# Performance work log

Hardware: AMD Instinct MI355X
Metric: run time of the kernel (lower is better)

The kernel has to match this reference:

```python
import jax, jax.numpy as jnp
import numpy as np

N = 50000      # num nodes
E = 1_600_000  # num edges
D = 64         # in_dim == hidden_dim
H = 4          # heads
C = 16         # head_dim = hidden_dim // heads
NEG = 0.2      # leaky_relu negative slope (PyG GATConv default)


def setup_inputs() -> dict:
    key = jax.random.key(0)
    ks = jax.random.split(key, 20)
    f = lambda k, s: (jax.random.normal(k, s, jnp.float32) * 0.1)
    return dict(
        node_features=jax.random.normal(ks[0], (N, D), jnp.float32),
        edge_index=jax.random.randint(ks[1], (2, E), 0, N, dtype=jnp.int32),
        edge_type=jax.random.randint(ks[2], (E,), 0, 5, dtype=jnp.int32),
        edge_attr=jax.random.normal(ks[3], (E, 1), jnp.float32),
        # GAT layer 1 (PyG GATConv: lin has no bias, att_* are [H,C], final bias [H*C])
        W1=f(ks[4], (D, H * C)), att_src1=f(ks[5], (H, C)), att_dst1=f(ks[6], (H, C)),
        We1=f(ks[7], (1, H * C)), att_e1=f(ks[8], (H, C)), b1=jnp.zeros((H * C,), jnp.float32),
        # GAT layer 2
        W2=f(ks[9], (D, H * C)), att_src2=f(ks[10], (H, C)), att_dst2=f(ks[11], (H, C)),
        We2=f(ks[12], (1, H * C)), att_e2=f(ks[13], (H, C)), b2=jnp.zeros((H * C,), jnp.float32),
        # LayerNorms
        g1=jnp.ones((D,), jnp.float32), beta1=jnp.zeros((D,), jnp.float32),
        g2=jnp.ones((D,), jnp.float32), beta2=jnp.zeros((D,), jnp.float32),
        # output head
        Wout=f(ks[14], (D, 1)), bout=jnp.zeros((1,), jnp.float32),
    )


def _layernorm(x, g, b, eps=1e-5):
    mu = x.mean(-1, keepdims=True)
    v = ((x - mu) ** 2).mean(-1, keepdims=True)
    return (x - mu) * jax.lax.rsqrt(v + eps) * g + b


def _seg_softmax(alpha, dst, n):
    # numerically stable segment softmax over incoming edges of each dst node
    m = jax.ops.segment_max(alpha, dst, num_segments=n)
    m = jnp.where(jnp.isfinite(m), m, 0.0)
    ex = jnp.exp(alpha - m[dst])
    den = jax.ops.segment_sum(ex, dst, num_segments=n)
    return ex / (den[dst] + 1e-16)


def _gatconv(x, src, dst, eattr, W, a_s, a_d, We, a_e, b, n):
    xs = (x @ W).reshape(n, H, C)                       # [N,H,C]
    a_src = jnp.einsum('nhc,hc->nh', xs, a_s)           # [N,H]
    a_dst = jnp.einsum('nhc,hc->nh', xs, a_d)           # [N,H]
    ee = (eattr @ We).reshape(-1, H, C)                 # [E',H,C]
    a_edge = jnp.einsum('ehc,hc->eh', ee, a_e)          # [E',H]
    alpha = a_src[src] + a_dst[dst] + a_edge            # [E',H]
    alpha = jax.nn.leaky_relu(alpha, NEG)
    alpha = _seg_softmax(alpha, dst, n)                 # [E',H]
    msg = xs[src] * alpha[..., None]                    # [E',H,C] gather-weighted messages
    out = jax.ops.segment_sum(msg, dst, num_segments=n) # scatter-aggregate
    return out.reshape(n, H * C) + b


def reference(node_features, edge_index, edge_type, edge_attr,
              W1, att_src1, att_dst1, We1, att_e1, b1,
              W2, att_src2, att_dst2, We2, att_e2, b2,
              g1, beta1, g2, beta2, Wout, bout):
    src, dst = edge_index[0], edge_index[1]
    # PyG add_self_loops(fill_value='mean'): self-loop edge_attr = mean of edge_attr over incoming edges
    cnt = jax.ops.segment_sum(jnp.ones((E,), jnp.float32), dst, num_segments=N)
    loop_attr = jax.ops.segment_sum(edge_attr, dst, num_segments=N) / jnp.maximum(cnt, 1.0)[:, None]
    loops = jnp.arange(N, dtype=src.dtype)
    src2 = jnp.concatenate([src, loops])
    dst2 = jnp.concatenate([dst, loops])
    ea = jnp.concatenate([edge_attr, loop_attr], axis=0)

    residual = node_features  # in_dim == hidden_dim -> no res_proj
    h = _gatconv(node_features, src2, dst2, ea, W1, att_src1, att_dst1, We1, att_e1, b1, N)
    h = jax.nn.elu(_layernorm(h + residual, g1, beta1))
    residual = h
    h = _gatconv(h, src2, dst2, ea, W2, att_src2, att_dst2, We2, att_e2, b2, N)
    h = jax.nn.elu(_layernorm(h + residual, g2, beta2))
    return h @ Wout + bout
```

## Files before the change

### kernel.cpp

```cpp
#include <hip/hip_runtime.h>
#include <hip/hip_bf16.h>
#include <cfloat>

#define NN 50000
#define NE 1600000
#define NEG 0.2f
#define NBKT 392
#define BNODE 128
#define P1_TILE 2048
#define P1_BLOCKS 782
#define CAP 16
#define BCAP 4608
#define SLOTS 96
#define L2E 1.4426950408889634f

typedef __attribute__((ext_vector_type(8))) short bf8_t;
typedef __attribute__((ext_vector_type(4))) float f4_t;

__device__ __forceinline__ float bf16bits_to_f(unsigned v) {
  return __uint_as_float(v << 16);
}
__device__ __forceinline__ unsigned f_to_bf16bits(float f) {
  unsigned u = __float_as_uint(f);
  return (u + 0x7fffu + ((u >> 16) & 1u)) >> 16;
}

__global__ __launch_bounds__(256) void bin_kernel(
    const int* __restrict__ src, const int* __restrict__ dst,
    const float* __restrict__ ea, int* __restrict__ gcnt,
    int2* __restrict__ gbuf) {
  __shared__ int lcnt[NBKT];
  __shared__ int lbase[NBKT];
  __shared__ int2 lbuf[NBKT][CAP];
  int t = threadIdx.x;
  for (int i = t; i < NBKT; i += 256) lcnt[i] = 0;
  __syncthreads();
  int e0 = blockIdx.x * P1_TILE;
#pragma unroll
  for (int k = 0; k < P1_TILE / 256; ++k) {
    int e = e0 + k * 256 + t;
    if (e < NE) {
      int d = dst[e];
      int b = d >> 7;
      int2 v = make_int2(((d & 127) << 16) | src[e], __float_as_int(ea[e]));
      int pos = atomicAdd(&lcnt[b], 1);
      if (pos < CAP) {
        lbuf[b][pos] = v;
      } else {
        int gp = atomicAdd(&gcnt[b], 1);
        if (gp < BCAP) gbuf[(size_t)b * BCAP + gp] = v;
      }
    }
  }
  __syncthreads();
  for (int i = t; i < NBKT; i += 256) {
    int len = lcnt[i]; if (len > CAP) len = CAP;
    lbase[i] = atomicAdd(&gcnt[i], len);
  }
  __syncthreads();
  for (int sid = t; sid < NBKT * CAP; sid += 256) {
    int b = sid >> 4;
    int k = sid & (CAP - 1);
    int len = lcnt[b]; if (len > CAP) len = CAP;
    if (k < len) {
      int base = lbase[b];
      if (base + k < BCAP) gbuf[(size_t)b * BCAP + base + k] = lbuf[b][k];
    }
  }
}

__global__ __launch_bounds__(256) void build_kernel(
    const int* __restrict__ gcnt, const int2* __restrict__ gbuf,
    int* __restrict__ cnt, unsigned* __restrict__ csr) {
  __shared__ int lc[BNODE];
  int t = threadIdx.x;
  int b = blockIdx.x;
  if (t < BNODE) lc[t] = 0;
  __syncthreads();
  int len = gcnt[b]; if (len > BCAP) len = BCAP;
  const int2* buf = gbuf + (size_t)b * BCAP;
  for (int i = t; i < len; i += 256) {
    int2 v = buf[i];
    int dl = (v.x >> 16) & 127;
    int s = v.x & 0xffff;
    int pos = atomicAdd(&lc[dl], 1);
    if (pos < SLOTS) {
      unsigned eb = ((unsigned)v.y) & 0xffff0000u;
      csr[(size_t)(b * BNODE + dl) * SLOTS + pos] = eb | (unsigned)s;
    }
  }
  __syncthreads();
  if (t < BNODE) {
    int n = b * BNODE + t;
    if (n < NN) cnt[n] = min(lc[t], SLOTS);
  }
}

__device__ __forceinline__ bf8_t pack8(const float* p) {
  bf8_t r;
#pragma unroll
  for (int i = 0; i < 8; ++i) r[i] = (short)f_to_bf16bits(p[i]);
  return r;
}

template <bool FP32IN>
__global__ __launch_bounds__(256) void gemm_mfma_kernel(
    const void* __restrict__ xin, const float* __restrict__ W,
    const float* __restrict__ att_s, const float* __restrict__ att_d,
    unsigned short* __restrict__ xsb, float* __restrict__ a_src,
    float* __restrict__ a_dst) {
  __shared__ unsigned short Wt[64][68];
  int t = threadIdx.x;
  for (int i = t; i < 4096; i += 256) {
    int k = i >> 6, n = i & 63;
    Wt[n][k] = (unsigned short)f_to_bf16bits(W[i]);
  }
  __syncthreads();
  int lane = t & 63, wave = t >> 6;
  int quad = lane >> 4, n16 = lane & 15;

  bf8_t bfrag[4][2];
#pragma unroll
  for (int nt = 0; nt < 4; ++nt)
#pragma unroll
    for (int kk = 0; kk < 2; ++kk)
      bfrag[nt][kk] = *(const bf8_t*)&Wt[nt * 16 + n16][kk * 32 + quad * 8];

  float as4[4], ad4[4];
#pragma unroll
  for (int nt = 0; nt < 4; ++nt) {
    as4[nt] = att_s[nt * 16 + n16];
    ad4[nt] = att_d[nt * 16 + n16];
  }

  int r0w = blockIdx.x * 128 + wave * 32;
#pragma unroll
  for (int tile = 0; tile < 2; ++tile) {
    int r0 = r0w + tile * 16;
    int rowA = r0 + n16; if (rowA > NN - 1) rowA = NN - 1;
    bf8_t af0, af1;
    if (FP32IN) {
      const float* xr = (const float*)xin + (size_t)rowA * 64 + quad * 8;
      af0 = pack8(xr);
      af1 = pack8(xr + 32);
    } else {
      const bf8_t* xrow =
          (const bf8_t*)((const unsigned short*)xin + (size_t)rowA * 64);
      af0 = xrow[quad];
      af1 = xrow[4 + quad];
    }
#pragma unroll
    for (int nt = 0; nt < 4; ++nt) {
      f4_t acc = {0.f, 0.f, 0.f, 0.f};
      acc = __builtin_amdgcn_mfma_f32_16x16x32_bf16(af0, bfrag[nt][0], acc, 0, 0, 0);
      acc = __builtin_amdgcn_mfma_f32_16x16x32_bf16(af1, bfrag[nt][1], acc, 0, 0, 0);
#pragma unroll
      for (int reg = 0; reg < 4; ++reg) {
        int row = r0 + quad * 4 + reg;
        float v = acc[reg];
        if (row < NN)
          xsb[(size_t)row * 64 + nt * 16 + n16] = (unsigned short)f_to_bf16bits(v);
        float p = v * as4[nt];
        float q = v * ad4[nt];
#pragma unroll
        for (int off = 8; off; off >>= 1) {
          p += __shfl_xor(p, off, 16);
          q += __shfl_xor(q, off, 16);
        }
        if (n16 == 0 && row < NN) {
          a_src[row * 4 + nt] = p * L2E;
          a_dst[row * 4 + nt] = q * L2E;
        }
      }
    }
  }
}

template <bool HEAD>
__global__ __launch_bounds__(256) void aggregate_kernel(
    const int* __restrict__ cnt, const unsigned* __restrict__ csr,
    const unsigned short* __restrict__ xsb, const float* __restrict__ a_src,
    const float* __restrict__ a_dst, const float* __restrict__ We,
    const float* __restrict__ att_e, const float* __restrict__ bias,
    const float* __restrict__ res, const float* __restrict__ g,
    const float* __restrict__ beta, const float* __restrict__ Wout,
    const float* __restrict__ bout, float* __restrict__ out,
    unsigned short* __restrict__ out_b) {
  __shared__ __align__(16) uint2 rec[4][64][4];
  int t = threadIdx.x;
  int lane = t & 63, wave = t >> 6;
  int n = blockIdx.x * 4 + wave;
  int d2 = lane & 31;
  int hb = d2 >> 3;
  int half = lane >> 5;

  float sp = We[lane] * att_e[lane];
#pragma unroll
  for (int off = 8; off; off >>= 1) sp += __shfl_xor(sp, off, 16);
  sp *= L2E;
  float s0 = __shfl(sp, 0, 64), s1 = __shfl(sp, 16, 64);
  float s2 = __shfl(sp, 32, 64), s3 = __shfl(sp, 48, 64);

  const float4 adv = *(const float4*)(a_dst + (size_t)n * 4);

  int dn = cnt[n];
  int r0 = n * SLOTS, r1 = r0 + dn;
  float accx = 0.f, accy = 0.f, den = 0.f, easum = 0.f;
  const uint2* rpb = &rec[wave][half][hb];
  const char* xd = (const char*)xsb + d2 * 4;

  for (int base = r0; base < r1; base += 64) {
    int c = r1 - base; if (c > 64) c = 64;
    int e = base + lane;
    unsigned ce = (e < r1) ? csr[e] : 0u;
    float ea = __uint_as_float(ce & 0xffff0000u);
    easum += ea;
    unsigned soff = (ce & 0xffffu) * 128u;
    float ex0 = 0.f, ex1 = 0.f, ex2 = 0.f, ex3 = 0.f;
    if (e < r1) {
      const float4 av = *(const float4*)(a_src + (size_t)(ce & 0xffffu) * 4);
      float a0 = av.x + fmaf(ea, s0, adv.x); a0 = fmaxf(a0, NEG * a0);
      float a1 = av.y + fmaf(ea, s1, adv.y); a1 = fmaxf(a1, NEG * a1);
      float a2 = av.z + fmaf(ea, s2, adv.z); a2 = fmaxf(a2, NEG * a2);
      float a3 = av.w + fmaf(ea, s3, adv.w); a3 = fmaxf(a3, NEG * a3);
      ex0 = exp2f(a0); ex1 = exp2f(a1); ex2 = exp2f(a2); ex3 = exp2f(a3);
    }
    uint4* wp = (uint4*)&rec[wave][lane][0];
    wp[0] = make_uint4(soff, __float_as_uint(ex0), soff, __float_as_uint(ex1));
    wp[1] = make_uint4(soff, __float_as_uint(ex2), soff, __float_as_uint(ex3));
    int c8 = (c + 7) & ~7;
    for (int j = 0; j < c8; j += 8) {
      uint2 va = rpb[j * 4];
      uint2 vb = rpb[j * 4 + 8];
      uint2 vc = rpb[j * 4 + 16];
      uint2 vd = rpb[j * 4 + 24];
      unsigned ua = *(const unsigned*)(xd + va.x);
      unsigned ub = *(const unsigned*)(xd + vb.x);
      unsigned uc = *(const unsigned*)(xd + vc.x);
      unsigned ud = *(const unsigned*)(xd + vd.x);
      float efa = __uint_as_float(va.y), efb = __uint_as_float(vb.y);
      float efc = __uint_as_float(vc.y), efd = __uint_as_float(vd.y);
      den += (efa + efb) + (efc + efd);
      accx = fmaf(efa, __uint_as_float(ua << 16), accx);
      accy = fmaf(efa, __uint_as_float(ua & 0xffff0000u), accy);
      accx = fmaf(efb, __uint_as_float(ub << 16), accx);
      accy = fmaf(efb, __uint_as_float(ub & 0xffff0000u), accy);
      accx = fmaf(efc, __uint_as_float(uc << 16), accx);
      accy = fmaf(efc, __uint_as_float(uc & 0xffff0000u), accy);
      accx = fmaf(efd, __uint_as_float(ud << 16), accx);
      accy = fmaf(efd, __uint_as_float(ud & 0xffff0000u), accy);
    }
  }

  den += __shfl_xor(den, 32, 64);
  accx += __shfl_xor(accx, 32, 64);
  accy += __shfl_xor(accy, 32, 64);
#pragma unroll
  for (int off = 32; off; off >>= 1) easum += __shfl_xor(easum, off, 64);

  float loop_ea = easum / fmaxf((float)dn, 1.0f);
  float as_h = a_src[(size_t)n * 4 + hb];
  float adn = (hb == 0) ? adv.x : (hb == 1) ? adv.y : (hb == 2) ? adv.z : adv.w;
  float sph = (hb == 0) ? s0 : (hb == 1) ? s1 : (hb == 2) ? s2 : s3;
  float a_self = as_h + fmaf(loop_ea, sph, adn);
  a_self = fmaxf(a_self, NEG * a_self);
  float ex_self = exp2f(a_self);
  den += ex_self;
  unsigned un = *(const unsigned*)((const char*)xsb + (size_t)n * 128 + d2 * 4);
  accx = fmaf(ex_self, __uint_as_float(un << 16), accx);
  accy = fmaf(ex_self, __uint_as_float(un & 0xffff0000u), accy);

  float rden = 1.f / (den + 1e-16f);
  const float2 bi = *(const float2*)(bias + d2 * 2);
  const float2 rsd = *(const float2*)(res + (size_t)n * 64 + d2 * 2);
  float vx = accx * rden + bi.x + rsd.x;
  float vy = accy * rden + bi.y + rsd.y;
  float s = vx + vy;
#pragma unroll
  for (int off = 32; off; off >>= 1) s += __shfl_xor(s, off, 64);
  float mu = s * (1.0f / 128.0f);
  float dx = vx - mu, dy = vy - mu;
  float var = dx * dx + dy * dy;
#pragma unroll
  for (int off = 32; off; off >>= 1) var += __shfl_xor(var, off, 64);
  var *= (1.0f / 128.0f);
  float rstd = rsqrtf(var + 1e-5f);
  const float2 gg = *(const float2*)(g + d2 * 2);
  const float2 bb = *(const float2*)(beta + d2 * 2);
  float yx = dx * rstd * gg.x + bb.x;
  float yy = dy * rstd * gg.y + bb.y;
  yx = yx > 0.f ? yx : expm1f(yx);
  yy = yy > 0.f ? yy : expm1f(yy);
  if (HEAD) {
    const float2 wv = *(const float2*)(Wout + d2 * 2);
    float p = yx * wv.x + yy * wv.y;
#pragma unroll
    for (int off = 32; off; off >>= 1) p += __shfl_xor(p, off, 64);
    if (lane == 0) out[n] = p * 0.5f + bout[0];
  } else if (lane < 32) {
    *(float2*)(out + (size_t)n * 64 + d2 * 2) = make_float2(yx, yy);
    unsigned ob = f_to_bf16bits(yx) | (f_to_bf16bits(yy) << 16);
    *(unsigned*)(out_b + (size_t)n * 64 + d2 * 2) = ob;
  }
}

extern "C" void kernel_launch(void* const* d_in, const int* in_sizes, int n_in,
                              void* d_out, int out_size, void* d_ws,
                              size_t ws_size, hipStream_t stream) {
  const float* node_features = (const float*)d_in[0];
  const int* edge_index = (const int*)d_in[1];
  const int* src = edge_index;
  const int* dst = edge_index + NE;
  const float* edge_attr = (const float*)d_in[3];
  const float* W1 = (const float*)d_in[4];
  const float* att_src1 = (const float*)d_in[5];
  const float* att_dst1 = (const float*)d_in[6];
  const float* We1 = (const float*)d_in[7];
  const float* att_e1 = (const float*)d_in[8];
  const float* b1 = (const float*)d_in[9];
  const float* W2 = (const float*)d_in[10];
  const float* att_src2 = (const float*)d_in[11];
  const float* att_dst2 = (const float*)d_in[12];
  const float* We2 = (const float*)d_in[13];
  const float* att_e2 = (const float*)d_in[14];
  const float* b2 = (const float*)d_in[15];
  const float* g1 = (const float*)d_in[16];
  const float* beta1 = (const float*)d_in[17];
  const float* g2 = (const float*)d_in[18];
  const float* beta2 = (const float*)d_in[19];
  const float* Wout = (const float*)d_in[20];
  const float* bout = (const float*)d_in[21];
  float* out = (float*)d_out;

  char* ws = (char*)d_ws;
  size_t o = 0;
  auto alloc = [&](size_t bytes) {
    void* p = ws + o;
    o += (bytes + 255) & ~(size_t)255;
    return p;
  };
  int* gcnt = (int*)alloc((size_t)NBKT * 4);
  int2* gbuf = (int2*)alloc((size_t)NBKT * BCAP * 8);
  int* cnt = (int*)alloc((size_t)NN * 4);
  unsigned* csr = (unsigned*)alloc((size_t)NN * SLOTS * 4);
  unsigned short* xsb = (unsigned short*)alloc((size_t)NN * 64 * 2);
  unsigned short* h1b = (unsigned short*)alloc((size_t)NN * 64 * 2);
  float* a_srcb = (float*)alloc((size_t)NN * 4 * 4);
  float* a_dstb = (float*)alloc((size_t)NN * 4 * 4);
  float* h1 = (float*)alloc((size_t)NN * 64 * 4);

  hipMemsetAsync(gcnt, 0, (size_t)NBKT * 4, stream);

  bin_kernel<<<P1_BLOCKS, 256, 0, stream>>>(src, dst, edge_attr, gcnt, gbuf);
  build_kernel<<<NBKT, 256, 0, stream>>>(gcnt, gbuf, cnt, csr);

  gemm_mfma_kernel<true><<<391, 256, 0, stream>>>(
      node_features, W1, att_src1, att_dst1, xsb, a_srcb, a_dstb);
  aggregate_kernel<false><<<NN / 4, 256, 0, stream>>>(
      cnt, csr, xsb, a_srcb, a_dstb, We1, att_e1, b1, node_features, g1, beta1,
      nullptr, nullptr, h1, h1b);

  gemm_mfma_kernel<false><<<391, 256, 0, stream>>>(
      h1b, W2, att_src2, att_dst2, xsb, a_srcb, a_dstb);
  aggregate_kernel<true><<<NN / 4, 256, 0, stream>>>(
      cnt, csr, xsb, a_srcb, a_dstb, We2, att_e2, b2, h1, g2, beta2, Wout, bout,
      out, nullptr);
}
```

Before: 268.0 us.

## Use two-pass count-then-scatter edge binning with smaller 64-node buckets

New measurement: 270.2 us. No clear change (+0.8%).

```diff
diff --git a/kernel.cpp b/kernel.cpp
--- a/kernel.cpp
+++ b/kernel.cpp
@@ -5,12 +5,11 @@
 #define NN 50000
 #define NE 1600000
 #define NEG 0.2f
-#define NBKT 392
-#define BNODE 128
+#define NBKT 782
+#define BNODE 64
 #define P1_TILE 2048
 #define P1_BLOCKS 782
-#define CAP 16
-#define BCAP 4608
+#define BCAP 2560
 #define SLOTS 96
 #define L2E 1.4426950408889634f
 
@@ -30,41 +29,33 @@
     const float* __restrict__ ea, int* __restrict__ gcnt,
     int2* __restrict__ gbuf) {
   __shared__ int lcnt[NBKT];
-  __shared__ int lbase[NBKT];
-  __shared__ int2 lbuf[NBKT][CAP];
+  __shared__ int lcur[NBKT];
   int t = threadIdx.x;
   for (int i = t; i < NBKT; i += 256) lcnt[i] = 0;
   __syncthreads();
   int e0 = blockIdx.x * P1_TILE;
-#pragma unroll
-  for (int k = 0; k < P1_TILE / 256; ++k) {
+  int bb[8], vx[8], vy[8];
+#pragma unroll
+  for (int k = 0; k < 8; ++k) {
     int e = e0 + k * 256 + t;
     if (e < NE) {
       int d = dst[e];
-      int b = d >> 7;
-      int2 v = make_int2(((d & 127) << 16) | src[e], __float_as_int(ea[e]));
-      int pos = atomicAdd(&lcnt[b], 1);
-      if (pos < CAP) {
-        lbuf[b][pos] = v;
-      } else {
-        int gp = atomicAdd(&gcnt[b], 1);
-        if (gp < BCAP) gbuf[(size_t)b * BCAP + gp] = v;
-      }
-    }
-  }
-  __syncthreads();
-  for (int i = t; i < NBKT; i += 256) {
-    int len = lcnt[i]; if (len > CAP) len = CAP;
-    lbase[i] = atomicAdd(&gcnt[i], len);
-  }
-  __syncthreads();
-  for (int sid = t; sid < NBKT * CAP; sid += 256) {
-    int b = sid >> 4;
-    int k = sid & (CAP - 1);
-    int len = lcnt[b]; if (len > CAP) len = CAP;
-    if (k < len) {
-      int base = lbase[b];
-      if (base + k < BCAP) gbuf[(size_t)b * BCAP + base + k] = lbuf[b][k];
+      bb[k] = d >> 6;
+      vx[k] = ((d & 63) << 16) | src[e];
+      vy[k] = __float_as_int(ea[e]);
+      atomicAdd(&lcnt[bb[k]], 1);
+    } else {
+      bb[k] = -1;
+    }
+  }
+  __syncthreads();
+  for (int i = t; i < NBKT; i += 256) lcur[i] = atomicAdd(&gcnt[i], lcnt[i]);
+  __syncthreads();
+#pragma unroll
+  for (int k = 0; k < 8; ++k) {
+    if (bb[k] >= 0) {
+      int pos = atomicAdd(&lcur[bb[k]], 1);
+      if (pos < BCAP) gbuf[(size_t)bb[k] * BCAP + pos] = make_int2(vx[k], vy[k]);
     }
   }
 }
@@ -81,7 +72,7 @@
   const int2* buf = gbuf + (size_t)b * BCAP;
   for (int i = t; i < len; i += 256) {
     int2 v = buf[i];
-    int dl = (v.x >> 16) & 127;
+    int dl = (v.x >> 16) & 63;
     int s = v.x & 0xffff;
     int pos = atomicAdd(&lc[dl], 1);
     if (pos < SLOTS) {
```
